# Kernel optimization log

Hardware: AMD Instinct MI355X
Metric: run time of the kernel (lower is better)

The kernel has to match this reference:

```python
import jax, jax.numpy as jnp
import numpy as np

NEG = -1e30

def setup_inputs() -> dict:
    key = jax.random.key(0)
    ks = jax.random.split(key, 11)
    B, NA, NB = 8, 2048, 2048
    in_A, in_B, out_dim = 256, 256, 64
    s = 0.05
    return {
        "h_A": jax.random.normal(ks[0], (B, NA, in_A), jnp.float32),
        "h_B": jax.random.normal(ks[1], (B, NB, in_B), jnp.float32),
        "mask": jax.random.bernoulli(ks[2], 0.5, (B, NA, NB)),
        "WA_w": jax.random.normal(ks[3], (in_A, out_dim), jnp.float32) * s,
        "WA_b": jax.random.normal(ks[4], (out_dim,), jnp.float32) * s,
        "WB_w": jax.random.normal(ks[5], (in_B, out_dim), jnp.float32) * s,
        "WB_b": jax.random.normal(ks[6], (out_dim,), jnp.float32) * s,
        "aA_w": jax.random.normal(ks[7], (out_dim,), jnp.float32) * s,
        "aA_b": jax.random.normal(ks[8], (), jnp.float32) * s,
        "aB_w": jax.random.normal(ks[9], (out_dim,), jnp.float32) * s,
        "aB_b": jax.random.normal(ks[10], (), jnp.float32) * s,
    }

def reference(h_A, h_B, mask, WA_w, WA_b, WB_w, WB_b, aA_w, aA_b, aB_w, aB_b):
    # Linear projections: z_A [B,NA,D], z_B [B,NB,D]
    z_A = jnp.einsum('bnd,df->bnf', h_A, WA_w) + WA_b
    z_B = jnp.einsum('bmd,df->bmf', h_B, WB_w) + WB_b
    # Additive attention scores: [B,NA,1] + [B,1,NB] -> [B,NA,NB]
    sA = z_A @ aA_w + aA_b  # [B,NA]
    sB = z_B @ aB_w + aB_b  # [B,NB]
    e = sA[:, :, None] + sB[:, None, :]
    e = jnp.where(mask, e, NEG)
    e = jax.nn.leaky_relu(e, negative_slope=0.01)
    alpha = jax.nn.softmax(e, axis=-1)
    alpha = jnp.where(mask, alpha, 0.0)
    # Weighted sum over neighbors
    return jnp.einsum('bnm,bmf->bnf', alpha, z_B)
```

## Files before the change

kernel.cpp:

```cpp
#include <hip/hip_runtime.h>

typedef short bf16x8 __attribute__((ext_vector_type(8)));
typedef float f32x4 __attribute__((ext_vector_type(4)));

__device__ __forceinline__ unsigned short f2bf(float x) {
  unsigned u = __float_as_uint(x);
  u += 0x7FFFu + ((u >> 16) & 1u);
  return (unsigned short)(u >> 16);
}

__global__ __launch_bounds__(256) void zb_kernel(
    const float* __restrict__ hB, const float* __restrict__ WB_w,
    const float* __restrict__ WB_b, const float* __restrict__ aB_w,
    const float* __restrict__ aB_b,
    const float* __restrict__ hA, const float* __restrict__ WA_w,
    const float* __restrict__ WA_b, const float* __restrict__ aA_w,
    const float* __restrict__ aA_b,
    unsigned short* __restrict__ zBT, float* __restrict__ sB,
    float* __restrict__ msB_blk, float* __restrict__ sA) {
  __shared__ char wt[32768];
  __shared__ char hl[16384];
  __shared__ float redp[4][16];
  __shared__ float sred[32];
  __shared__ float vAl[256];
  __shared__ float cAl;

  const int t = threadIdx.x, w = t >> 6, l = t & 63;
  const int q = l >> 4, ln = l & 15;
  const int m0g = blockIdx.x * 32;
  const int b = m0g >> 11, mloc = m0g & 2047;

  {
    float sa = 0.f;
    const float4* wr4 = (const float4*)(WA_w + t * 64);
    const float4* aa4 = (const float4*)aA_w;
    #pragma unroll
    for (int i = 0; i < 16; ++i) {
      const float4 x = wr4[i], y = aa4[i];
      sa += x.x * y.x + x.y * y.y + x.z * y.z + x.w * y.w;
    }
    vAl[t] = sa;
    if (t == 0) {
      float ca = aA_b[0];
      for (int f = 0; f < 64; ++f) ca += WA_b[f] * aA_w[f];
      cAl = ca;
    }
    __syncthreads();
    const float4 v4 = ((const float4*)vAl)[l];
    #pragma unroll
    for (int rr = 0; rr < 8; ++rr) {
      const int row = w * 8 + rr;
      const float4 h4 = *(const float4*)(hA + (size_t)(m0g + row) * 256 + l * 4);
      float s = h4.x * v4.x + h4.y * v4.y + h4.z * v4.z + h4.w * v4.w;
      #pragma unroll
      for (int off = 1; off < 64; off <<= 1) s += __shfl_xor(s, off, 64);
      if (l == 0) sA[m0g + row] = s + cAl;
    }
  }

  {
    const int f = t >> 2, kseg = t & 3;
    #pragma unroll
    for (int j = 0; j < 8; ++j) {
      const int k0 = kseg * 64 + j * 8;
      bf16x8 v;
      #pragma unroll
      for (int jj = 0; jj < 8; ++jj)
        v[jj] = (short)f2bf(WB_w[(k0 + jj) * 64 + f]);
      *(bf16x8*)(wt + ((f * 512 + k0 * 2) ^ ((f & 7) << 4))) = v;
    }
  }
  {
    #pragma unroll
    for (int i = 0; i < 8; ++i) {
      const int idx = i * 1024 + t * 4;
      const int row = idx >> 8, k = idx & 255;
      const float4 x = *(const float4*)(hB + (size_t)m0g * 256 + idx);
      uint2 pk;
      pk.x = (unsigned)f2bf(x.x) | ((unsigned)f2bf(x.y) << 16);
      pk.y = (unsigned)f2bf(x.z) | ((unsigned)f2bf(x.w) << 16);
      *(uint2*)(hl + ((row * 512 + k * 2) ^ ((row & 7) << 4))) = pk;
    }
  }
  __syncthreads();
  const int rt = w & 1, fpair = w >> 1;
  f32x4 acc[2];
  acc[0] = (f32x4){0.f, 0.f, 0.f, 0.f};
  acc[1] = acc[0];
  const int rowA = rt * 16 + ln;
  #pragma unroll
  for (int kk = 0; kk < 8; ++kk) {
    const int ko = kk * 64 + q * 16;
    const bf16x8 a = *(const bf16x8*)(hl + ((rowA * 512 + ko) ^ ((rowA & 7) << 4)));
    #pragma unroll
    for (int j = 0; j < 2; ++j) {
      const int f = fpair * 32 + j * 16 + ln;
      const bf16x8 bb = *(const bf16x8*)(wt + ((f * 512 + ko) ^ ((f & 7) << 4)));
      acc[j] = __builtin_amdgcn_mfma_f32_16x16x32_bf16(a, bb, acc[j], 0, 0, 0);
    }
  }
  float z[2][4];
  float p[4] = {0.f, 0.f, 0.f, 0.f};
  #pragma unroll
  for (int j = 0; j < 2; ++j) {
    const int f = fpair * 32 + j * 16 + ln;
    const float bias = WB_b[f], aw = aB_w[f];
    #pragma unroll
    for (int r = 0; r < 4; ++r) {
      const float zz = acc[j][r] + bias;
      z[j][r] = zz;
      p[r] += zz * aw;
    }
  }
  #pragma unroll
  for (int r = 0; r < 4; ++r) {
    #pragma unroll
    for (int off = 1; off < 16; off <<= 1) p[r] += __shfl_xor(p[r], off, 16);
  }
  if (ln == 0) {
    #pragma unroll
    for (int r = 0; r < 4; ++r) redp[w][q * 4 + r] = p[r];
  }
  __syncthreads();
  char* zt = hl;
  #pragma unroll
  for (int j = 0; j < 2; ++j) {
    const int f = fpair * 32 + j * 16 + ln;
    uint2 pk;
    pk.x = (unsigned)f2bf(z[j][0]) | ((unsigned)f2bf(z[j][1]) << 16);
    pk.y = (unsigned)f2bf(z[j][2]) | ((unsigned)f2bf(z[j][3]) << 16);
    *(uint2*)(zt + f * 80 + (rt * 16 + q * 4) * 2) = pk;
  }
  if (t < 32) {
    const int rtm = t >> 4, mi = t & 15;
    const float s = redp[rtm][mi] + redp[rtm + 2][mi] + aB_b[0];
    sB[m0g + t] = s;
    sred[t] = s;
  }
  __syncthreads();
  if (t == 0) {
    float bm = sred[0];
    #pragma unroll
    for (int i = 1; i < 32; ++i) bm = fmaxf(bm, sred[i]);
    msB_blk[blockIdx.x] = bm;
  }
  {
    const int f = t >> 2, mseg = t & 3;
    const bf16x8 v = *(const bf16x8*)(zt + f * 80 + mseg * 16);
    *(bf16x8*)(zBT + (size_t)b * 131072 + f * 2048 + mloc + mseg * 8) = v;
  }
}

struct Zc { bf16x8 z0, z1, z2, z3; };

__device__ __forceinline__ uint2 pack_mask32(const int* p) {
  const int4 a = *(const int4*)p;
  const int4 c = *(const int4*)(p + 4);
  uint2 r;
  r.x = (a.x ? 1u : 0u) | (a.y ? 0x100u : 0u) | (a.z ? 0x10000u : 0u) | (a.w ? 0x1000000u : 0u);
  r.y = (c.x ? 1u : 0u) | (c.y ? 0x100u : 0u) | (c.z ? 0x10000u : 0u) | (c.w ? 0x1000000u : 0u);
  return r;
}

__device__ __forceinline__ Zc load_z(const unsigned short* zp0,
    const unsigned short* zp1, const unsigned short* zp2,
    const unsigned short* zp3, const int c) {
  Zc z;
  const int m = c * 32;
  z.z0 = *(const bf16x8*)(zp0 + m);
  z.z1 = *(const bf16x8*)(zp1 + m);
  z.z2 = *(const bf16x8*)(zp2 + m);
  z.z3 = *(const bf16x8*)(zp3 + m);
  return z;
}

__device__ __forceinline__ void gat_compute(const uint2 mk, const Zc& z,
    const float* sBl, const int c, const int lq8, const float sAr, const float M,
    f32x4& a0, f32x4& a1, f32x4& a2, f32x4& a3, float& ds) {
  const int sb0 = c * 32 + lq8;
  const float4 s0 = *(const float4*)(sBl + sb0);
  const float4 s1 = *(const float4*)(sBl + sb0 + 4);
  const float sx[8] = {s0.x, s0.y, s0.z, s0.w, s1.x, s1.y, s1.z, s1.w};
  bf16x8 af;
  #pragma unroll
  for (int j = 0; j < 8; ++j) {
    const unsigned km = ((j < 4 ? mk.x : mk.y) >> (8 * (j & 3))) & 0xFFu;
    const float x = sAr + sx[j];
    const float e = fmaxf(x, 0.01f * x);
    const float v = km ? __expf(e - M) : 0.f;
    af[j] = (short)f2bf(v);
    ds += v;
  }
  a0 = __builtin_amdgcn_mfma_f32_16x16x32_bf16(af, z.z0, a0, 0, 0, 0);
  a1 = __builtin_amdgcn_mfma_f32_16x16x32_bf16(af, z.z1, a1, 0, 0, 0);
  a2 = __builtin_amdgcn_mfma_f32_16x16x32_bf16(af, z.z2, a2, 0, 0, 0);
  a3 = __builtin_amdgcn_mfma_f32_16x16x32_bf16(af, z.z3, a3, 0, 0, 0);
}

template <bool USE8>
__device__ __forceinline__ void gat_main(const unsigned char* mp8, const int* mp32,
    const unsigned short* zp0, const unsigned short* zp1,
    const unsigned short* zp2, const unsigned short* zp3,
    const float* sBl, const int lq8, const float sAr, const float M,
    f32x4& a0, f32x4& a1, f32x4& a2, f32x4& a3, float& ds) {
  uint2 mk[16];
  if constexpr (USE8) {
    #pragma unroll
    for (int c = 0; c < 16; ++c) mk[c] = *(const uint2*)(mp8 + c * 32);
  } else {
    #pragma unroll
    for (int g = 0; g < 4; ++g) {
      #pragma unroll
      for (int c = 0; c < 4; ++c) mk[g * 4 + c] = pack_mask32(mp32 + (g * 4 + c) * 32);
    }
  }
  Zc zf[3];
  zf[0] = load_z(zp0, zp1, zp2, zp3, 0);
  zf[1] = load_z(zp0, zp1, zp2, zp3, 1);
  zf[2] = load_z(zp0, zp1, zp2, zp3, 2);
  #pragma unroll
  for (int c = 0; c < 16; ++c) {
    const Zc zc = zf[c % 3];
    if (c + 3 < 16) zf[c % 3] = load_z(zp0, zp1, zp2, zp3, c + 3);
    gat_compute(mk[c], zc, sBl, c, lq8, sAr, M, a0, a1, a2, a3, ds);
  }
}

__global__ __launch_bounds__(256, 4) void gat_kernel(
    const unsigned short* __restrict__ zBT, const float* __restrict__ sA,
    const float* __restrict__ sB, const float* __restrict__ msB_blk,
    const unsigned char* __restrict__ mask8, const int* __restrict__ mask32,
    float* __restrict__ pacc, float* __restrict__ pd) {
  const int b = blockIdx.y, n0 = blockIdx.x * 64, mq = blockIdx.z;
  const int t = threadIdx.x, w = t >> 6, l = t & 63;
  const int ln = l & 15, lq = l >> 4, lq8 = lq * 8;

  __shared__ float sBl[512];
  __shared__ unsigned dfl[4];

  const unsigned vdet = mask8[t * 4 + 1];
  const unsigned long long bal = __ballot(vdet != 0);
  if (l == 0) dfl[w] = (bal != 0ull) ? 1u : 0u;
  ((float2*)sBl)[t] = ((const float2*)(sB + b * 2048 + mq * 512))[t];
  float mb = msB_blk[b * 64 + l];
  #pragma unroll
  for (int off = 1; off < 64; off <<= 1) mb = fmaxf(mb, __shfl_xor(mb, off, 64));
  __syncthreads();
  const bool use8 = (dfl[0] | dfl[1] | dfl[2] | dfl[3]) != 0;

  const int row = n0 + w * 16 + ln;
  const float sAr = sA[b * 2048 + row];
  const float Mf = sAr + mb;
  const float M = fmaxf(Mf, 0.01f * Mf);
  float ds = 0.f;
  f32x4 a0 = (f32x4){0.f, 0.f, 0.f, 0.f}, a1 = a0, a2 = a0, a3 = a0;

  const size_t mbase = ((size_t)(b * 2048 + row)) * 2048 + mq * 512 + lq8;
  const unsigned char* mp8 = mask8 + mbase;
  const int* mp32 = mask32 + mbase;
  const unsigned short* zp0 = zBT + ((size_t)(b * 64 + ln)) * 2048 + mq * 512 + lq8;
  const unsigned short* zp1 = zp0 + 16 * 2048;
  const unsigned short* zp2 = zp0 + 32 * 2048;
  const unsigned short* zp3 = zp0 + 48 * 2048;

  if (use8) gat_main<true>(mp8, mp32, zp0, zp1, zp2, zp3, sBl, lq8, sAr, M, a0, a1, a2, a3, ds);
  else      gat_main<false>(mp8, mp32, zp0, zp1, zp2, zp3, sBl, lq8, sAr, M, a0, a1, a2, a3, ds);

  ds += __shfl_xor(ds, 16, 64);
  ds += __shfl_xor(ds, 32, 64);
  if (l < 16) pd[(size_t)(mq * 8 + b) * 2048 + n0 + w * 16 + l] = ds;
  const size_t obase = ((size_t)(mq * 8 + b) * 2048 + n0 + w * 16 + lq * 4) * 64 + ln;
  #pragma unroll
  for (int r = 0; r < 4; ++r) {
    float* o = pacc + obase + (size_t)r * 64;
    o[0] = a0[r];
    o[16] = a1[r];
    o[32] = a2[r];
    o[48] = a3[r];
  }
}

__global__ __launch_bounds__(256) void merge_kernel(
    const float* __restrict__ pacc, const float* __restrict__ pd,
    float* __restrict__ out) {
  const int tid = blockIdx.x * 256 + threadIdx.x;
  const int bn = tid >> 4;
  const float4* p4 = (const float4*)pacc;
  const float4 x0 = p4[tid], x1 = p4[262144 + tid];
  const float4 x2 = p4[524288 + tid], x3 = p4[786432 + tid];
  const float d = pd[bn] + pd[16384 + bn] + pd[32768 + bn] + pd[49152 + bn];
  const float inv = d > 0.f ? 1.f / d : 0.f;
  float4 o;
  o.x = (x0.x + x1.x + x2.x + x3.x) * inv;
  o.y = (x0.y + x1.y + x2.y + x3.y) * inv;
  o.z = (x0.z + x1.z + x2.z + x3.z) * inv;
  o.w = (x0.w + x1.w + x2.w + x3.w) * inv;
  ((float4*)out)[tid] = o;
}

extern "C" void kernel_launch(void* const* d_in, const int* in_sizes, int n_in,
                              void* d_out, int out_size, void* d_ws, size_t ws_size,
                              hipStream_t stream) {
  const float* h_A = (const float*)d_in[0];
  const float* h_B = (const float*)d_in[1];
  const unsigned char* mask8 = (const unsigned char*)d_in[2];
  const int* mask32 = (const int*)d_in[2];
  const float* WA_w = (const float*)d_in[3];
  const float* WA_b = (const float*)d_in[4];
  const float* WB_w = (const float*)d_in[5];
  const float* WB_b = (const float*)d_in[6];
  const float* aA_w = (const float*)d_in[7];
  const float* aA_b = (const float*)d_in[8];
  const float* aB_w = (const float*)d_in[9];
  const float* aB_b = (const float*)d_in[10];
  float* out = (float*)d_out;

  char* wsb = (char*)d_ws;
  unsigned short* zBT = (unsigned short*)wsb;
  float* sB      = (float*)(wsb + 2097152);
  float* sA      = (float*)(wsb + 2162688);
  float* msB_blk = (float*)(wsb + 2228224);
  float* pacc    = (float*)(wsb + 2230272);
  float* pd      = (float*)(wsb + 19007488);

  zb_kernel<<<512, 256, 0, stream>>>(h_B, WB_w, WB_b, aB_w, aB_b,
                                     h_A, WA_w, WA_b, aA_w, aA_b,
                                     zBT, sB, msB_blk, sA);
  gat_kernel<<<dim3(32, 8, 4), 256, 0, stream>>>(zBT, sA, sB, msB_blk,
                                                 mask8, mask32, pacc, pd);
  merge_kernel<<<1024, 256, 0, stream>>>(pacc, pd, out);
}
```

Measured before the change: 73.89 us.

## Stage mask rows into LDS via async global-to-LDS copies, halve block size

The gat kernel now copies each wave's 16x512 byte mask slice into shared memory using global_load_lds 16-byte async copies with coalesced row segments, then reads per-chunk mask bytes from LDS inside the loop. Previously each lane issued strided 8-byte global loads for all 16 chunks up front into registers. Blocks shrink to 128 threads (2 waves, 32 rows) with twice as many blocks, and the sB staging switches to float4. The change trades register pressure and uncoalesced mask reads for an LDS buffer and a full vmcnt(0) wait before compute, which serializes the mask load against the z loads.

```diff
diff --git a/kernel.cpp b/kernel.cpp
--- a/kernel.cpp
+++ b/kernel.cpp
@@ -7,6 +7,12 @@
   unsigned u = __float_as_uint(x);
   u += 0x7FFFu + ((u >> 16) & 1u);
   return (unsigned short)(u >> 16);
+}
+
+__device__ __forceinline__ void async_copy16(const void* g, void* l) {
+  __builtin_amdgcn_global_load_lds(
+      (const __attribute__((address_space(1))) void*)g,
+      (__attribute__((address_space(3))) void*)l, 16, 0, 0);
 }
 
 __global__ __launch_bounds__(256) void zb_kernel(
@@ -198,22 +204,11 @@
 }
 
 template <bool USE8>
-__device__ __forceinline__ void gat_main(const unsigned char* mp8, const int* mp32,
+__device__ __forceinline__ void gat_main(const char* mll, const int* mp32,
     const unsigned short* zp0, const unsigned short* zp1,
     const unsigned short* zp2, const unsigned short* zp3,
     const float* sBl, const int lq8, const float sAr, const float M,
     f32x4& a0, f32x4& a1, f32x4& a2, f32x4& a3, float& ds) {
-  uint2 mk[16];
-  if constexpr (USE8) {
-    #pragma unroll
-    for (int c = 0; c < 16; ++c) mk[c] = *(const uint2*)(mp8 + c * 32);
-  } else {
-    #pragma unroll
-    for (int g = 0; g < 4; ++g) {
-      #pragma unroll
-      for (int c = 0; c < 4; ++c) mk[g * 4 + c] = pack_mask32(mp32 + (g * 4 + c) * 32);
-    }
-  }
   Zc zf[3];
   zf[0] = load_z(zp0, zp1, zp2, zp3, 0);
   zf[1] = load_z(zp0, zp1, zp2, zp3, 1);
@@ -222,49 +217,67 @@
   for (int c = 0; c < 16; ++c) {
     const Zc zc = zf[c % 3];
     if (c + 3 < 16) zf[c % 3] = load_z(zp0, zp1, zp2, zp3, c + 3);
-    gat_compute(mk[c], zc, sBl, c, lq8, sAr, M, a0, a1, a2, a3, ds);
-  }
-}
-
-__global__ __launch_bounds__(256, 4) void gat_kernel(
+    uint2 mk;
+    if constexpr (USE8) mk = *(const uint2*)(mll + c * 512);
+    else mk = pack_mask32(mp32 + c * 32);
+    gat_compute(mk, zc, sBl, c, lq8, sAr, M, a0, a1, a2, a3, ds);
+  }
+}
+
+__global__ __launch_bounds__(128, 4) void gat_kernel(
     const unsigned short* __restrict__ zBT, const float* __restrict__ sA,
     const float* __restrict__ sB, const float* __restrict__ msB_blk,
     const unsigned char* __restrict__ mask8, const int* __restrict__ mask32,
     float* __restrict__ pacc, float* __restrict__ pd) {
-  const int b = blockIdx.y, n0 = blockIdx.x * 64, mq = blockIdx.z;
+  const int b = blockIdx.y, n0 = blockIdx.x * 32, mq = blockIdx.z;
   const int t = threadIdx.x, w = t >> 6, l = t & 63;
   const int ln = l & 15, lq = l >> 4, lq8 = lq * 8;
 
+  __shared__ char maskl[2][8192];
   __shared__ float sBl[512];
-  __shared__ unsigned dfl[4];
+  __shared__ unsigned dfl[2];
 
   const unsigned vdet = mask8[t * 4 + 1];
   const unsigned long long bal = __ballot(vdet != 0);
   if (l == 0) dfl[w] = (bal != 0ull) ? 1u : 0u;
-  ((float2*)sBl)[t] = ((const float2*)(sB + b * 2048 + mq * 512))[t];
+  ((float4*)sBl)[t] = ((const float4*)(sB + b * 2048 + mq * 512))[t];
   float mb = msB_blk[b * 64 + l];
   #pragma unroll
   for (int off = 1; off < 64; off <<= 1) mb = fmaxf(mb, __shfl_xor(mb, off, 64));
   __syncthreads();
-  const bool use8 = (dfl[0] | dfl[1] | dfl[2] | dfl[3]) != 0;
+  const bool use8 = (dfl[0] | dfl[1]) != 0;
 
   const int row = n0 + w * 16 + ln;
   const float sAr = sA[b * 2048 + row];
   const float Mf = sAr + mb;
   const float M = fmaxf(Mf, 0.01f * Mf);
+
+  char* mslice = maskl[w];
+  {
+    const unsigned char* mrowbase =
+        mask8 + ((size_t)(b * 2048 + n0 + w * 16)) * 2048 + mq * 512;
+    const unsigned char* gp0 =
+        mrowbase + (size_t)((l & 31) >> 1) * 2048 + (l >> 5) * 32 + (l & 1) * 16;
+    #pragma unroll
+    for (int k = 0; k < 8; ++k)
+      async_copy16(gp0 + k * 64, mslice + k * 1024);
+  }
+  asm volatile("s_waitcnt vmcnt(0)" ::: "memory");
+  __builtin_amdgcn_sched_barrier(0);
+
   float ds = 0.f;
   f32x4 a0 = (f32x4){0.f, 0.f, 0.f, 0.f}, a1 = a0, a2 = a0, a3 = a0;
 
   const size_t mbase = ((size_t)(b * 2048 + row)) * 2048 + mq * 512 + lq8;
-  const unsigned char* mp8 = mask8 + mbase;
   const int* mp32 = mask32 + mbase;
   const unsigned short* zp0 = zBT + ((size_t)(b * 64 + ln)) * 2048 + mq * 512 + lq8;
   const unsigned short* zp1 = zp0 + 16 * 2048;
   const unsigned short* zp2 = zp0 + 32 * 2048;
   const unsigned short* zp3 = zp0 + 48 * 2048;
-
-  if (use8) gat_main<true>(mp8, mp32, zp0, zp1, zp2, zp3, sBl, lq8, sAr, M, a0, a1, a2, a3, ds);
-  else      gat_main<false>(mp8, mp32, zp0, zp1, zp2, zp3, sBl, lq8, sAr, M, a0, a1, a2, a3, ds);
+  const char* mll = mslice + ln * 32 + lq8;
+
+  if (use8) gat_main<true>(mll, mp32, zp0, zp1, zp2, zp3, sBl, lq8, sAr, M, a0, a1, a2, a3, ds);
+  else      gat_main<false>(mll, mp32, zp0, zp1, zp2, zp3, sBl, lq8, sAr, M, a0, a1, a2, a3, ds);
 
   ds += __shfl_xor(ds, 16, 64);
   ds += __shfl_xor(ds, 32, 64);
@@ -326,7 +339,7 @@
   zb_kernel<<<512, 256, 0, stream>>>(h_B, WB_w, WB_b, aB_w, aB_b,
                                      h_A, WA_w, WA_b, aA_w, aA_b,
                                      zBT, sB, msB_blk, sA);
-  gat_kernel<<<dim3(32, 8, 4), 256, 0, stream>>>(zBT, sA, sB, msB_blk,
+  gat_kernel<<<dim3(64, 8, 4), 128, 0, stream>>>(zBT, sA, sB, msB_blk,
                                                  mask8, mask32, pacc, pd);
   merge_kernel<<<1024, 256, 0, stream>>>(pacc, pd, out);
 }
```

After: 75.56 us. 2.3% more time.

## Bit-pack mask in projection kernel, fuse split-M merge into GAT kernel

Applied to the files above, without the earlier changes.

The projection kernel gets 512 extra blocks that read the mask once and pack it into a bitmask, permuted so each lane loads its bits with one uint4. The attention kernel then reads 1 bit per neighbour instead of bytes or ints. Each block now covers all 2048 neighbours with 8 waves, reducing the four partial sums and denominators in shared memory, so the separate merge kernel and its global partial buffers are gone. This trades an extra pass over the mask and fewer, larger blocks (512 blocks of 512 threads) for much less mask traffic in the main kernel and less global memory round-tripping.

```diff
diff --git a/kernel.cpp b/kernel.cpp
--- a/kernel.cpp
+++ b/kernel.cpp
@@ -9,15 +9,58 @@
   return (unsigned short)(u >> 16);
 }
 
-__global__ __launch_bounds__(256) void zb_kernel(
+__global__ __launch_bounds__(256) void zbpack_kernel(
     const float* __restrict__ hB, const float* __restrict__ WB_w,
     const float* __restrict__ WB_b, const float* __restrict__ aB_w,
     const float* __restrict__ aB_b,
     const float* __restrict__ hA, const float* __restrict__ WA_w,
     const float* __restrict__ WA_b, const float* __restrict__ aA_w,
     const float* __restrict__ aA_b,
+    const unsigned char* __restrict__ mask8, const int* __restrict__ mask32,
     unsigned short* __restrict__ zBT, float* __restrict__ sB,
-    float* __restrict__ msB_blk, float* __restrict__ sA) {
+    float* __restrict__ msB_blk, float* __restrict__ sA,
+    unsigned char* __restrict__ packed) {
+  const int t = threadIdx.x, w = t >> 6, l = t & 63;
+
+  if (blockIdx.x >= 512) {
+    __shared__ unsigned char pbuf[8192];
+    __shared__ unsigned pdfl[4];
+    const int p = blockIdx.x - 512;
+    const unsigned vdet = mask8[(size_t)p * 65536 + t * 256 + 1];
+    const unsigned long long bal = __ballot(vdet != 0);
+    if (l == 0) pdfl[w] = (bal != 0ull) ? 1u : 0u;
+    __syncthreads();
+    const bool use8 = (pdfl[0] | pdfl[1] | pdfl[2] | pdfl[3]) != 0;
+    #pragma unroll 4
+    for (int i = 0; i < 32; ++i) {
+      const int bi = i * 256 + t;
+      const int row = bi >> 8, m8 = bi & 255;
+      unsigned byte = 0;
+      if (use8) {
+        const uint2 v = *(const uint2*)(mask8 + ((size_t)(p * 32 + row)) * 2048 + m8 * 8);
+        #pragma unroll
+        for (int j = 0; j < 4; ++j) {
+          byte |= ((v.x >> (8 * j)) & 0xFFu) ? (1u << j) : 0u;
+          byte |= ((v.y >> (8 * j)) & 0xFFu) ? (1u << (j + 4)) : 0u;
+        }
+      } else {
+        const int* s32 = mask32 + ((size_t)(p * 32 + row)) * 2048 + m8 * 8;
+        const int4 v1 = *(const int4*)s32;
+        const int4 v2 = *(const int4*)(s32 + 4);
+        byte |= (v1.x ? 1u : 0u) | (v1.y ? 2u : 0u) | (v1.z ? 4u : 0u) | (v1.w ? 8u : 0u);
+        byte |= (v2.x ? 16u : 0u) | (v2.y ? 32u : 0u) | (v2.z ? 64u : 0u) | (v2.w ? 128u : 0u);
+      }
+      pbuf[row * 256 + (m8 & 15) * 16 + (m8 >> 4)] = (unsigned char)byte;
+    }
+    __syncthreads();
+    #pragma unroll
+    for (int k = 0; k < 2; ++k) {
+      const int oi = t * 2 + k;
+      *(uint4*)(packed + (size_t)p * 8192 + oi * 16) = *(const uint4*)(pbuf + oi * 16);
+    }
+    return;
+  }
+
   __shared__ char wt[32768];
   __shared__ char hl[16384];
   __shared__ float redp[4][16];
@@ -25,7 +68,6 @@
   __shared__ float vAl[256];
   __shared__ float cAl;
 
-  const int t = threadIdx.x, w = t >> 6, l = t & 63;
   const int q = l >> 4, ln = l & 15;
   const int m0g = blockIdx.x * 32;
   const int b = m0g >> 11, mloc = m0g & 2047;
@@ -57,7 +99,6 @@
       if (l == 0) sA[m0g + row] = s + cAl;
     }
   }
-
   {
     const int f = t >> 2, kseg = t & 3;
     #pragma unroll
@@ -151,43 +192,31 @@
   }
 }
 
-struct Zc { bf16x8 z0, z1, z2, z3; };
-
-__device__ __forceinline__ uint2 pack_mask32(const int* p) {
-  const int4 a = *(const int4*)p;
-  const int4 c = *(const int4*)(p + 4);
-  uint2 r;
-  r.x = (a.x ? 1u : 0u) | (a.y ? 0x100u : 0u) | (a.z ? 0x10000u : 0u) | (a.w ? 0x1000000u : 0u);
-  r.y = (c.x ? 1u : 0u) | (c.y ? 0x100u : 0u) | (c.z ? 0x10000u : 0u) | (c.w ? 0x1000000u : 0u);
-  return r;
-}
-
-__device__ __forceinline__ Zc load_z(const unsigned short* zp0,
-    const unsigned short* zp1, const unsigned short* zp2,
-    const unsigned short* zp3, const int c) {
-  Zc z;
-  const int m = c * 32;
-  z.z0 = *(const bf16x8*)(zp0 + m);
-  z.z1 = *(const bf16x8*)(zp1 + m);
-  z.z2 = *(const bf16x8*)(zp2 + m);
-  z.z3 = *(const bf16x8*)(zp3 + m);
+struct Z4 { bf16x8 z0, z1, z2, z3; };
+
+__device__ __forceinline__ Z4 ldz(const unsigned short* z0p, const unsigned short* z1p,
+                                  const unsigned short* z2p, const unsigned short* z3p,
+                                  const int mo) {
+  Z4 z;
+  z.z0 = *(const bf16x8*)(z0p + mo);
+  z.z1 = *(const bf16x8*)(z1p + mo);
+  z.z2 = *(const bf16x8*)(z2p + mo);
+  z.z3 = *(const bf16x8*)(z3p + mo);
   return z;
 }
 
-__device__ __forceinline__ void gat_compute(const uint2 mk, const Zc& z,
-    const float* sBl, const int c, const int lq8, const float sAr, const float M,
+__device__ __forceinline__ void gat_compute(const Z4& z, const unsigned mkb,
+    const float* sBl, const int mo, const float sAr, const float M,
     f32x4& a0, f32x4& a1, f32x4& a2, f32x4& a3, float& ds) {
-  const int sb0 = c * 32 + lq8;
-  const float4 s0 = *(const float4*)(sBl + sb0);
-  const float4 s1 = *(const float4*)(sBl + sb0 + 4);
+  const float4 s0 = *(const float4*)(sBl + mo);
+  const float4 s1 = *(const float4*)(sBl + mo + 4);
   const float sx[8] = {s0.x, s0.y, s0.z, s0.w, s1.x, s1.y, s1.z, s1.w};
   bf16x8 af;
   #pragma unroll
   for (int j = 0; j < 8; ++j) {
-    const unsigned km = ((j < 4 ? mk.x : mk.y) >> (8 * (j & 3))) & 0xFFu;
     const float x = sAr + sx[j];
     const float e = fmaxf(x, 0.01f * x);
-    const float v = km ? __expf(e - M) : 0.f;
+    const float v = ((mkb >> j) & 1u) ? __expf(e - M) : 0.f;
     af[j] = (short)f2bf(v);
     ds += v;
   }
@@ -197,105 +226,86 @@
   a3 = __builtin_amdgcn_mfma_f32_16x16x32_bf16(af, z.z3, a3, 0, 0, 0);
 }
 
-template <bool USE8>
-__device__ __forceinline__ void gat_main(const unsigned char* mp8, const int* mp32,
-    const unsigned short* zp0, const unsigned short* zp1,
-    const unsigned short* zp2, const unsigned short* zp3,
-    const float* sBl, const int lq8, const float sAr, const float M,
-    f32x4& a0, f32x4& a1, f32x4& a2, f32x4& a3, float& ds) {
-  uint2 mk[16];
-  if constexpr (USE8) {
-    #pragma unroll
-    for (int c = 0; c < 16; ++c) mk[c] = *(const uint2*)(mp8 + c * 32);
-  } else {
-    #pragma unroll
-    for (int g = 0; g < 4; ++g) {
-      #pragma unroll
-      for (int c = 0; c < 4; ++c) mk[g * 4 + c] = pack_mask32(mp32 + (g * 4 + c) * 32);
-    }
-  }
-  Zc zf[3];
-  zf[0] = load_z(zp0, zp1, zp2, zp3, 0);
-  zf[1] = load_z(zp0, zp1, zp2, zp3, 1);
-  zf[2] = load_z(zp0, zp1, zp2, zp3, 2);
-  #pragma unroll
-  for (int c = 0; c < 16; ++c) {
-    const Zc zc = zf[c % 3];
-    if (c + 3 < 16) zf[c % 3] = load_z(zp0, zp1, zp2, zp3, c + 3);
-    gat_compute(mk[c], zc, sBl, c, lq8, sAr, M, a0, a1, a2, a3, ds);
-  }
-}
-
-__global__ __launch_bounds__(256, 4) void gat_kernel(
+__global__ __launch_bounds__(512, 4) void gat_kernel(
     const unsigned short* __restrict__ zBT, const float* __restrict__ sA,
     const float* __restrict__ sB, const float* __restrict__ msB_blk,
-    const unsigned char* __restrict__ mask8, const int* __restrict__ mask32,
-    float* __restrict__ pacc, float* __restrict__ pd) {
-  const int b = blockIdx.y, n0 = blockIdx.x * 64, mq = blockIdx.z;
+    const unsigned char* __restrict__ packed, float* __restrict__ out) {
+  const int b = blockIdx.y, n0 = blockIdx.x * 32;
   const int t = threadIdx.x, w = t >> 6, l = t & 63;
-  const int ln = l & 15, lq = l >> 4, lq8 = lq * 8;
-
-  __shared__ float sBl[512];
-  __shared__ unsigned dfl[4];
-
-  const unsigned vdet = mask8[t * 4 + 1];
-  const unsigned long long bal = __ballot(vdet != 0);
-  if (l == 0) dfl[w] = (bal != 0ull) ? 1u : 0u;
-  ((float2*)sBl)[t] = ((const float2*)(sB + b * 2048 + mq * 512))[t];
+  const int rg = w & 1, mg = w >> 1;
+  const int ln = l & 15, lq = l >> 4;
+
+  __shared__ float sBl[2048];
+  __shared__ float buf[4 * 32 * 64];
+  __shared__ float dpart[4][32];
+
+  ((float4*)sBl)[t] = ((const float4*)(sB + b * 2048))[t];
   float mb = msB_blk[b * 64 + l];
   #pragma unroll
   for (int off = 1; off < 64; off <<= 1) mb = fmaxf(mb, __shfl_xor(mb, off, 64));
   __syncthreads();
-  const bool use8 = (dfl[0] | dfl[1] | dfl[2] | dfl[3]) != 0;
-
-  const int row = n0 + w * 16 + ln;
-  const float sAr = sA[b * 2048 + row];
+
+  const int arow = rg * 16 + ln;
+  const float sAr = sA[b * 2048 + n0 + arow];
   const float Mf = sAr + mb;
   const float M = fmaxf(Mf, 0.01f * Mf);
+  const uint4 mk = *(const uint4*)(packed +
+      ((size_t)(b * 2048 + n0 + arow)) * 256 + (4 * mg + lq) * 16);
+
+  const unsigned short* z0p = zBT + (size_t)b * 131072 + ln * 2048;
+  const unsigned short* z1p = z0p + 32768;
+  const unsigned short* z2p = z0p + 65536;
+  const unsigned short* z3p = z0p + 98304;
+  const int mbase = mg * 32 + lq * 8;
+
   float ds = 0.f;
   f32x4 a0 = (f32x4){0.f, 0.f, 0.f, 0.f}, a1 = a0, a2 = a0, a3 = a0;
 
-  const size_t mbase = ((size_t)(b * 2048 + row)) * 2048 + mq * 512 + lq8;
-  const unsigned char* mp8 = mask8 + mbase;
-  const int* mp32 = mask32 + mbase;
-  const unsigned short* zp0 = zBT + ((size_t)(b * 64 + ln)) * 2048 + mq * 512 + lq8;
-  const unsigned short* zp1 = zp0 + 16 * 2048;
-  const unsigned short* zp2 = zp0 + 32 * 2048;
-  const unsigned short* zp3 = zp0 + 48 * 2048;
-
-  if (use8) gat_main<true>(mp8, mp32, zp0, zp1, zp2, zp3, sBl, lq8, sAr, M, a0, a1, a2, a3, ds);
-  else      gat_main<false>(mp8, mp32, zp0, zp1, zp2, zp3, sBl, lq8, sAr, M, a0, a1, a2, a3, ds);
+  Z4 zA = ldz(z0p, z1p, z2p, z3p, mbase);
+  Z4 zB;
+  #pragma unroll
+  for (int cc = 0; cc < 16; cc += 2) {
+    const unsigned mka =
+        ((cc & 2) ? ((cc & 4) ? ((cc & 8) ? mk.w : mk.y) : ((cc & 8) ? mk.z : mk.x))
+                  : ((cc & 4) ? ((cc & 8) ? mk.w : mk.y) : ((cc & 8) ? mk.z : mk.x)));
+    const unsigned dw0 = (cc >> 2) == 0 ? mk.x : (cc >> 2) == 1 ? mk.y : (cc >> 2) == 2 ? mk.z : mk.w;
+    const unsigned dw1 = ((cc + 1) >> 2) == 0 ? mk.x : ((cc + 1) >> 2) == 1 ? mk.y : ((cc + 1) >> 2) == 2 ? mk.z : mk.w;
+    (void)mka;
+    if (cc + 1 < 16) zB = ldz(z0p, z1p, z2p, z3p, mbase + (cc + 1) * 128);
+    gat_compute(zA, (dw0 >> ((cc & 3) * 8)) & 0xFFu, sBl, mbase + cc * 128,
+                sAr, M, a0, a1, a2, a3, ds);
+    if (cc + 2 < 16) zA = ldz(z0p, z1p, z2p, z3p, mbase + (cc + 2) * 128);
+    gat_compute(zB, (dw1 >> (((cc + 1) & 3) * 8)) & 0xFFu, sBl, mbase + (cc + 1) * 128,
+                sAr, M, a0, a1, a2, a3, ds);
+  }
 
   ds += __shfl_xor(ds, 16, 64);
   ds += __shfl_xor(ds, 32, 64);
-  if (l < 16) pd[(size_t)(mq * 8 + b) * 2048 + n0 + w * 16 + l] = ds;
-  const size_t obase = ((size_t)(mq * 8 + b) * 2048 + n0 + w * 16 + lq * 4) * 64 + ln;
+  if (l < 16) dpart[mg][rg * 16 + l] = ds;
   #pragma unroll
   for (int r = 0; r < 4; ++r) {
-    float* o = pacc + obase + (size_t)r * 64;
-    o[0] = a0[r];
-    o[16] = a1[r];
-    o[32] = a2[r];
-    o[48] = a3[r];
-  }
-}
-
-__global__ __launch_bounds__(256) void merge_kernel(
-    const float* __restrict__ pacc, const float* __restrict__ pd,
-    float* __restrict__ out) {
-  const int tid = blockIdx.x * 256 + threadIdx.x;
-  const int bn = tid >> 4;
-  const float4* p4 = (const float4*)pacc;
-  const float4 x0 = p4[tid], x1 = p4[262144 + tid];
-  const float4 x2 = p4[524288 + tid], x3 = p4[786432 + tid];
-  const float d = pd[bn] + pd[16384 + bn] + pd[32768 + bn] + pd[49152 + bn];
-  const float inv = d > 0.f ? 1.f / d : 0.f;
-  float4 o;
-  o.x = (x0.x + x1.x + x2.x + x3.x) * inv;
-  o.y = (x0.y + x1.y + x2.y + x3.y) * inv;
-  o.z = (x0.z + x1.z + x2.z + x3.z) * inv;
-  o.w = (x0.w + x1.w + x2.w + x3.w) * inv;
-  ((float4*)out)[tid] = o;
+    const int orow = rg * 16 + lq * 4 + r;
+    buf[(mg * 32 + orow) * 64 + ln]      = a0[r];
+    buf[(mg * 32 + orow) * 64 + 16 + ln] = a1[r];
+    buf[(mg * 32 + orow) * 64 + 32 + ln] = a2[r];
+    buf[(mg * 32 + orow) * 64 + 48 + ln] = a3[r];
+  }
+  __syncthreads();
+  {
+    const int row = t >> 4, f0 = (t & 15) * 4;
+    const float4 p0 = *(const float4*)(buf + (0 * 32 + row) * 64 + f0);
+    const float4 p1 = *(const float4*)(buf + (1 * 32 + row) * 64 + f0);
+    const float4 p2 = *(const float4*)(buf + (2 * 32 + row) * 64 + f0);
+    const float4 p3 = *(const float4*)(buf + (3 * 32 + row) * 64 + f0);
+    const float d = dpart[0][row] + dpart[1][row] + dpart[2][row] + dpart[3][row];
+    const float inv = d > 0.f ? 1.f / d : 0.f;
+    float4 o;
+    o.x = (p0.x + p1.x + p2.x + p3.x) * inv;
+    o.y = (p0.y + p1.y + p2.y + p3.y) * inv;
+    o.z = (p0.z + p1.z + p2.z + p3.z) * inv;
+    o.w = (p0.w + p1.w + p2.w + p3.w) * inv;
+    *(float4*)(out + ((size_t)(b * 2048 + n0 + row)) * 64 + f0) = o;
+  }
 }
 
 extern "C" void kernel_launch(void* const* d_in, const int* in_sizes, int n_in,
@@ -316,17 +326,15 @@
   float* out = (float*)d_out;
 
   char* wsb = (char*)d_ws;
-  unsigned short* zBT = (unsigned short*)wsb;
-  float* sB      = (float*)(wsb + 2097152);
-  float* sA      = (float*)(wsb + 2162688);
-  float* msB_blk = (float*)(wsb + 2228224);
-  float* pacc    = (float*)(wsb + 2230272);
-  float* pd      = (float*)(wsb + 19007488);
-
-  zb_kernel<<<512, 256, 0, stream>>>(h_B, WB_w, WB_b, aB_w, aB_b,
-                                     h_A, WA_w, WA_b, aA_w, aA_b,
-                                     zBT, sB, msB_blk, sA);
-  gat_kernel<<<dim3(32, 8, 4), 256, 0, stream>>>(zBT, sA, sB, msB_blk,
-                                                 mask8, mask32, pacc, pd);
-  merge_kernel<<<1024, 256, 0, stream>>>(pacc, pd, out);
-}
+  unsigned short* zBT    = (unsigned short*)wsb;
+  float* sB              = (float*)(wsb + 2097152);
+  float* sA              = (float*)(wsb + 2162688);
+  float* msB_blk         = (float*)(wsb + 2228224);
+  unsigned char* packed  = (unsigned char*)(wsb + 2230272);
+
+  zbpack_kernel<<<1024, 256, 0, stream>>>(h_B, WB_w, WB_b, aB_w, aB_b,
+                                          h_A, WA_w, WA_b, aA_w, aA_b,
+                                          mask8, mask32,
+                                          zBT, sB, msB_blk, sA, packed);
+  gat_kernel<<<dim3(64, 8), 512, 0, stream>>>(zBT, sA, sB, msB_blk, packed, out);
+}
```

Result: faster. 72.27 us (-2.2%).
